# Optimization experiments

Measured on AMD Instinct MI355X. Metric: run time of the kernel, lower is better.

The kernel has to match this reference:

```python
import jax, jax.numpy as jnp
import numpy as np
from math import comb

ORDER = 16
K = ORDER + 1  # 17
D = 32         # input_dim
P = 20         # num_perm
N = 24576


def _bernstein(X, order):
    # X: [N, D] in [0,1] -> Bernstein basis [N, D, order+1]
    ks = jnp.arange(order + 1)
    binoms = jnp.array([comb(order, k) for k in range(order + 1)], jnp.float32)
    Xe = X[..., None]
    return (Xe ** ks) * ((1.0 - Xe) ** (order - ks)) * binoms


def _prior_sc_np(order):
    # prior_adjusting: sqrt(inv(B(x)^2) @ 1) at x = linspace(0,1,order+1)
    ks = np.arange(order + 1)
    binoms = np.array([comb(order, k) for k in range(order + 1)], np.float64)
    x = np.linspace(0.0, 1.0, order + 1)[:, None]
    B = (x ** ks) * ((1.0 - x) ** (order - ks)) * binoms  # (K, K)
    Pmat = np.linalg.inv(B ** 2)
    v = Pmat @ np.ones((order + 1, 1))
    return np.sqrt(np.maximum(v, 1e-12)).astype(np.float32)  # (K, 1)


def setup_inputs() -> dict:
    key = jax.random.key(0)
    k1, k2, k3, k4, k5 = jax.random.split(key, 5)
    mean_mu = (0.0001 / P) ** (1.0 / D)
    Xnew = jax.random.uniform(k1, (N, D), dtype=jnp.float32)
    meanw0 = mean_mu + 0.1 * jax.random.normal(k2, (P, 1, K), dtype=jnp.float32)
    meanw = mean_mu + 0.1 * jax.random.normal(k3, (D - 1, P, K, K), dtype=jnp.float32)
    varw0 = -0.1 + 0.1 * jax.random.normal(k4, (P, 1, K), dtype=jnp.float32)
    varw = -0.1 + 0.1 * jax.random.normal(k5, (D - 1, P, K, K), dtype=jnp.float32)
    rng = np.random.default_rng(0)
    perm = jnp.array(np.stack([rng.permutation(D) for _ in range(P)]), jnp.int32)
    prior_sc = jnp.array(_prior_sc_np(ORDER))
    post_prec = jnp.full((P,), float(P), dtype=jnp.float32)
    return {"Xnew": Xnew, "meanw0": meanw0, "meanw": meanw, "varw0": varw0,
            "varw": varw, "prior_sc": prior_sc, "post_prec": post_prec, "perm": perm}


def reference(Xnew, meanw0, meanw, varw0, varw, prior_sc, post_prec, perm):
    Bout = _bernstein(Xnew, ORDER)                      # (N, D, K)
    outB = jnp.transpose(Bout[:, perm], (1, 0, 2, 3))   # (P, N, D, K)
    outBd = jnp.transpose(outB, (2, 0, 1, 3))           # (D, P, N, K)

    # f_mean: ones(P,N,1) @ meanw0 -> broadcast of meanw0 rows; then chained small matmuls
    f0 = meanw0[:, 0, :][:, None, :] * outBd[0]         # (P, N, K)

    def mean_step(f, inputs):
        W, b = inputs                                   # W: (P,K,K), b: (P,N,K)
        return jnp.einsum('pnk,pkj->pnj', f, W) * b, None

    f, _ = jax.lax.scan(mean_step, f0, (meanw, outBd[1:]))
    f_mean = jnp.sum(jnp.sum(f, axis=-1), axis=0)[:, None]  # (N, 1)

    # f_var: weights exp(varw)*prior_sc^2.T, basis squared
    sc2 = (prior_sc ** 2)[:, 0]                          # (K,)
    g0 = (jnp.exp(varw0) * sc2)[:, 0, :][:, None, :] * outBd[0] ** 2  # (P, N, K)

    def var_step(g, inputs):
        Vw, b = inputs
        return jnp.einsum('pnk,pkj->pnj', g, jnp.exp(Vw) * sc2) * (b ** 2), None

    g, _ = jax.lax.scan(var_step, g0, (varw, outBd[1:]))
    f_var = jnp.sum(jnp.sum(g, axis=-1) / post_prec[:, None], axis=0)[:, None]  # (N, 1)
    return f_mean, f_var
```

## Files before the change

### kernel.cpp

```cpp
#include <hip/hip_runtime.h>

#define NN 24576
#define DD 32
#define KK 17
#define PP 20

__device__ __forceinline__ void bern17(float x, float* b) {
    const float binom[KK] = {1.f, 16.f, 120.f, 560.f, 1820.f, 4368.f, 8008.f, 11440.f,
                             12870.f, 11440.f, 8008.f, 4368.f, 1820.f, 560.f, 120.f, 16.f, 1.f};
    const float y = 1.0f - x;
    b[0] = 1.0f;
#pragma unroll
    for (int k = 1; k < KK; ++k) b[k] = b[k - 1] * x;
    float yp = 1.0f;
#pragma unroll
    for (int k = KK - 1; k >= 0; --k) {
        b[k] = b[k] * yp * binom[k];
        yp *= y;
    }
}

__global__ void prep_var(const float* __restrict__ varw, const float* __restrict__ varw0,
                         const float* __restrict__ prior_sc,
                         float* __restrict__ wv, float* __restrict__ wv0) {
    const int E1 = (DD - 1) * PP * KK * KK;
    int idx = blockIdx.x * blockDim.x + threadIdx.x;
    if (idx < E1) {
        int j = idx % KK;
        float s = prior_sc[j];
        wv[idx] = expf(varw[idx]) * s * s;
    } else if (idx < E1 + PP * KK) {
        int i = idx - E1;
        int k = i % KK;
        float s = prior_sc[k];
        wv0[i] = expf(varw0[i]) * s * s;
    }
}

__global__ void transpose_x(const float* __restrict__ X, float* __restrict__ XT) {
    __shared__ float t[32][33];
    const int n0 = blockIdx.x * 32;
    for (int r = threadIdx.y; r < 32; r += 8)
        t[r][threadIdx.x] = X[(n0 + r) * DD + threadIdx.x];
    __syncthreads();
    for (int d = threadIdx.y; d < 32; d += 8)
        XT[d * NN + n0 + threadIdx.x] = t[threadIdx.x][d];
}

__global__ __launch_bounds__(256, 4) void bez_chain2x2(
    const float* __restrict__ Xb,
    const float* __restrict__ mw0,
    const float* __restrict__ mW,
    const float* __restrict__ vw0,
    const float* __restrict__ vW,
    const float* __restrict__ post_prec,
    const int* __restrict__ perm,
    float* __restrict__ out)
{
    const bool VAR = (blockIdx.z != 0);
    const int p = blockIdx.y;
    const int n0 = blockIdx.x * 512 + threadIdx.x;
    const int n1 = n0 + 256;
    const int* __restrict__ pp = perm + p * DD;

    const float* __restrict__ w0 = (VAR ? vw0 : mw0);
    const float* __restrict__ W  = (VAR ? vW  : mW);

    float f0[KK], f1[KK], b0[KK], b1[KK];

    {
        const int pd = pp[0];
        const float x0 = Xb[pd * NN + n0];
        const float x1 = Xb[pd * NN + n1];
        bern17(x0, b0);
        bern17(x1, b1);
        if (VAR) {
#pragma unroll
            for (int k = 0; k < KK; ++k) { b0[k] *= b0[k]; b1[k] *= b1[k]; }
        }
        const float* __restrict__ w0p = w0 + p * KK;
#pragma unroll
        for (int k = 0; k < KK; ++k) { f0[k] = w0p[k] * b0[k]; f1[k] = w0p[k] * b1[k]; }
    }

    for (int d = 1; d < DD; ++d) {
        const int pd = pp[d];
        const float x0 = Xb[pd * NN + n0];
        const float x1 = Xb[pd * NN + n1];
        bern17(x0, b0);
        bern17(x1, b1);
        if (VAR) {
#pragma unroll
            for (int k = 0; k < KK; ++k) { b0[k] *= b0[k]; b1[k] *= b1[k]; }
        }

        const float* __restrict__ Wd = W + ((size_t)(d - 1) * PP + p) * (KK * KK);

        float fn0[KK], fn1[KK];
#pragma unroll
        for (int j = 0; j < KK; ++j) {
            const float w = Wd[j];
            fn0[j] = f0[0] * w;
            fn1[j] = f1[0] * w;
        }
#pragma unroll
        for (int k = 1; k < KK; ++k) {
            const float fk0 = f0[k];
            const float fk1 = f1[k];
#pragma unroll
            for (int j = 0; j < KK; ++j) {
                const float w = Wd[k * KK + j];
                fn0[j] = fmaf(fk0, w, fn0[j]);
                fn1[j] = fmaf(fk1, w, fn1[j]);
            }
        }
#pragma unroll
        for (int j = 0; j < KK; ++j) { f0[j] = fn0[j] * b0[j]; f1[j] = fn1[j] * b1[j]; }
    }

    float s0 = 0.0f, s1 = 0.0f;
#pragma unroll
    for (int j = 0; j < KK; ++j) { s0 += f0[j]; s1 += f1[j]; }
    if (VAR) { const float ip = 1.0f / post_prec[p]; s0 *= ip; s1 *= ip; }

    const int base = VAR ? NN : 0;
    atomicAdd(&out[base + n0], s0);
    atomicAdd(&out[base + n1], s1);
}

__global__ __launch_bounds__(256, 4) void bez_chain2(
    const float* __restrict__ Xb, const int sx_d, const int sx_n,
    const float* __restrict__ mw0, const float* __restrict__ mW,
    const float* __restrict__ vw0, const float* __restrict__ vW,
    const float* __restrict__ post_prec, const int* __restrict__ perm,
    float* __restrict__ out)
{
    const bool VAR = (blockIdx.z != 0);
    const int p = blockIdx.y;
    const int n = blockIdx.x * blockDim.x + threadIdx.x;
    const int* __restrict__ pp = perm + p * DD;
    const float* __restrict__ w0 = (VAR ? vw0 : mw0);
    const float* __restrict__ W  = (VAR ? vW  : mW);

    float f[KK], b[KK];
    {
        const int pd = pp[0];
        const float x = Xb[pd * sx_d + n * sx_n];
        bern17(x, b);
        if (VAR) {
#pragma unroll
            for (int k = 0; k < KK; ++k) b[k] *= b[k];
        }
        const float* __restrict__ w0p = w0 + p * KK;
#pragma unroll
        for (int k = 0; k < KK; ++k) f[k] = w0p[k] * b[k];
    }
    for (int d = 1; d < DD; ++d) {
        const int pd = pp[d];
        const float x = Xb[pd * sx_d + n * sx_n];
        bern17(x, b);
        if (VAR) {
#pragma unroll
            for (int k = 0; k < KK; ++k) b[k] *= b[k];
        }
        const float* __restrict__ Wd = W + ((size_t)(d - 1) * PP + p) * (KK * KK);
        float fn[KK];
#pragma unroll
        for (int j = 0; j < KK; ++j) fn[j] = 0.0f;
#pragma unroll
        for (int k = 0; k < KK; ++k) {
            const float fk = f[k];
#pragma unroll
            for (int j = 0; j < KK; ++j)
                fn[j] = fmaf(fk, Wd[k * KK + j], fn[j]);
        }
#pragma unroll
        for (int j = 0; j < KK; ++j) f[j] = fn[j] * b[j];
    }
    float s = 0.0f;
#pragma unroll
    for (int j = 0; j < KK; ++j) s += f[j];
    if (VAR) s /= post_prec[p];
    atomicAdd(&out[(VAR ? NN : 0) + n], s);
}

extern "C" void kernel_launch(void* const* d_in, const int* in_sizes, int n_in,
                              void* d_out, int out_size, void* d_ws, size_t ws_size,
                              hipStream_t stream) {
    const float* X    = (const float*)d_in[0];
    const float* mw0  = (const float*)d_in[1];
    const float* mw   = (const float*)d_in[2];
    const float* vw0  = (const float*)d_in[3];
    const float* vw   = (const float*)d_in[4];
    const float* psc  = (const float*)d_in[5];
    const float* ppr  = (const float*)d_in[6];
    const int*   perm = (const int*)d_in[7];
    float* out = (float*)d_out;

    const size_t wv_elems  = (size_t)(DD - 1) * PP * KK * KK;
    const size_t wv0_elems = (size_t)PP * KK;
    const size_t xt_elems  = (size_t)DD * NN;

    float* wv  = (float*)d_ws;
    float* wv0 = wv + wv_elems;
    float* XT  = wv0 + wv0_elems;

    const size_t need = (wv_elems + wv0_elems + xt_elems) * sizeof(float);
    const bool use_xt = (ws_size >= need);

    hipMemsetAsync(d_out, 0, (size_t)out_size * sizeof(float), stream);

    const int E = (DD - 1) * PP * KK * KK + PP * KK;
    prep_var<<<dim3((E + 255) / 256), dim3(256), 0, stream>>>(vw, vw0, psc, wv, wv0);

    if (use_xt) {
        transpose_x<<<dim3(NN / 32), dim3(32, 8), 0, stream>>>(X, XT);
        dim3 grid(NN / 512, PP, 2), blk(256);
        bez_chain2x2<<<grid, blk, 0, stream>>>(XT, mw0, mw, wv0, wv, ppr, perm, out);
    } else {
        dim3 grid(NN / 256, PP, 2), blk(256);
        bez_chain2<<<grid, blk, 0, stream>>>(X, 1, DD, mw0, mw, wv0, wv, ppr, perm, out);
    }
}
```

Measured before the change: 286.8 us.

## Fold binomial coefficients into weights and process four points per thread

The binomial coefficients of the Bernstein basis are moved out of the per-point basis evaluation and folded into the weight matrices, columnwise, in a prep kernel that now handles both the mean and variance weights. The main kernel now computes four points per thread instead of two, so each weight load is reused across more FMAs. The basis evaluation is placed after the matrix product to shorten live ranges. Occupancy is lowered to two blocks per CU to give room for the larger register footprint, which risks spilling or less latency hiding.

Result: slower. 879.1 us (+206.5%).

```diff
diff --git a/kernel.cpp b/kernel.cpp
--- a/kernel.cpp
+++ b/kernel.cpp
@@ -4,10 +4,169 @@
 #define DD 32
 #define KK 17
 #define PP 20
+#define WEU ((DD - 1) * PP * KK * KK)
+
+__device__ __forceinline__ float binom16(int k) {
+    const float b[KK] = {1.f, 16.f, 120.f, 560.f, 1820.f, 4368.f, 8008.f, 11440.f,
+                         12870.f, 11440.f, 8008.f, 4368.f, 1820.f, 560.f, 120.f, 16.f, 1.f};
+    return b[k];
+}
+
+__device__ __forceinline__ void bernT(float x, float* t) {
+    const float y = 1.0f - x;
+    t[0] = 1.0f;
+#pragma unroll
+    for (int k = 1; k < KK; ++k) t[k] = t[k - 1] * x;
+    float yp = y;
+#pragma unroll
+    for (int k = KK - 2; k >= 0; --k) {
+        t[k] *= yp;
+        yp *= y;
+    }
+}
+
+__global__ void prep_w_fold(const float* __restrict__ mw, const float* __restrict__ vw,
+                            const float* __restrict__ mw0, const float* __restrict__ vw0,
+                            const float* __restrict__ psc,
+                            float* __restrict__ Wm2, float* __restrict__ Wv2,
+                            float* __restrict__ w0m, float* __restrict__ w0v) {
+    int idx = blockIdx.x * blockDim.x + threadIdx.x;
+    if (idx < WEU) {
+        const int j = idx % KK;
+        Wm2[idx] = mw[idx] * binom16(j);
+    } else if (idx < 2 * WEU) {
+        const int i = idx - WEU;
+        const int j = i % KK;
+        const float s = psc[j] * binom16(j);
+        Wv2[i] = expf(vw[i]) * s * s;
+    } else if (idx < 2 * WEU + PP * KK) {
+        const int i = idx - 2 * WEU;
+        const int k = i % KK;
+        w0m[i] = mw0[i] * binom16(k);
+    } else if (idx < 2 * WEU + 2 * PP * KK) {
+        const int i = idx - 2 * WEU - PP * KK;
+        const int k = i % KK;
+        const float s = psc[k] * binom16(k);
+        w0v[i] = expf(vw0[i]) * s * s;
+    }
+}
+
+__global__ void transpose_x(const float* __restrict__ X, float* __restrict__ XT) {
+    __shared__ float t[32][33];
+    const int n0 = blockIdx.x * 32;
+    for (int r = threadIdx.y; r < 32; r += 8)
+        t[r][threadIdx.x] = X[(n0 + r) * DD + threadIdx.x];
+    __syncthreads();
+    for (int d = threadIdx.y; d < 32; d += 8)
+        XT[d * NN + n0 + threadIdx.x] = t[threadIdx.x][d];
+}
+
+__global__ __launch_bounds__(256, 2) void bez_chain4x(
+    const float* __restrict__ Xb,
+    const float* __restrict__ w0m,
+    const float* __restrict__ mW,
+    const float* __restrict__ w0v,
+    const float* __restrict__ vW,
+    const float* __restrict__ post_prec,
+    const int* __restrict__ perm,
+    float* __restrict__ out)
+{
+    const bool VAR = (blockIdx.z != 0);
+    const int p = blockIdx.y;
+    const int n0 = blockIdx.x * 1024 + threadIdx.x;
+    const int* __restrict__ pp = perm + p * DD;
+
+    const float* __restrict__ w0 = (VAR ? w0v : w0m);
+    const float* __restrict__ W  = (VAR ? vW  : mW);
+
+    float f0[KK], f1[KK], f2[KK], f3[KK];
+
+    {
+        const int pd = pp[0];
+        const float* __restrict__ xr = Xb + (size_t)pd * NN + n0;
+        float b0[KK], b1[KK], b2[KK], b3[KK];
+        bernT(xr[0], b0);
+        bernT(xr[256], b1);
+        bernT(xr[512], b2);
+        bernT(xr[768], b3);
+        if (VAR) {
+#pragma unroll
+            for (int k = 0; k < KK; ++k) {
+                b0[k] *= b0[k]; b1[k] *= b1[k]; b2[k] *= b2[k]; b3[k] *= b3[k];
+            }
+        }
+        const float* __restrict__ w0p = w0 + p * KK;
+#pragma unroll
+        for (int k = 0; k < KK; ++k) {
+            const float w = w0p[k];
+            f0[k] = w * b0[k]; f1[k] = w * b1[k]; f2[k] = w * b2[k]; f3[k] = w * b3[k];
+        }
+    }
+
+    for (int d = 1; d < DD; ++d) {
+        const int pd = pp[d];
+        const float* __restrict__ xr = Xb + (size_t)pd * NN + n0;
+        const float x0 = xr[0];
+        const float x1 = xr[256];
+        const float x2 = xr[512];
+        const float x3 = xr[768];
+
+        const float* __restrict__ Wd = W + ((size_t)(d - 1) * PP + p) * (KK * KK);
+
+        float fn0[KK], fn1[KK], fn2[KK], fn3[KK];
+#pragma unroll
+        for (int j = 0; j < KK; ++j) {
+            const float w = Wd[j];
+            fn0[j] = f0[0] * w; fn1[j] = f1[0] * w;
+            fn2[j] = f2[0] * w; fn3[j] = f3[0] * w;
+        }
+#pragma unroll
+        for (int k = 1; k < KK; ++k) {
+            const float a0 = f0[k], a1 = f1[k], a2 = f2[k], a3 = f3[k];
+#pragma unroll
+            for (int j = 0; j < KK; ++j) {
+                const float w = Wd[k * KK + j];
+                fn0[j] = fmaf(a0, w, fn0[j]);
+                fn1[j] = fmaf(a1, w, fn1[j]);
+                fn2[j] = fmaf(a2, w, fn2[j]);
+                fn3[j] = fmaf(a3, w, fn3[j]);
+            }
+        }
+
+        float b0[KK], b1[KK], b2[KK], b3[KK];
+        bernT(x0, b0);
+        bernT(x1, b1);
+        bernT(x2, b2);
+        bernT(x3, b3);
+        if (VAR) {
+#pragma unroll
+            for (int k = 0; k < KK; ++k) {
+                b0[k] *= b0[k]; b1[k] *= b1[k]; b2[k] *= b2[k]; b3[k] *= b3[k];
+            }
+        }
+#pragma unroll
+        for (int j = 0; j < KK; ++j) {
+            f0[j] = fn0[j] * b0[j]; f1[j] = fn1[j] * b1[j];
+            f2[j] = fn2[j] * b2[j]; f3[j] = fn3[j] * b3[j];
+        }
+    }
+
+    float s0 = 0.0f, s1 = 0.0f, s2 = 0.0f, s3 = 0.0f;
+#pragma unroll
+    for (int j = 0; j < KK; ++j) { s0 += f0[j]; s1 += f1[j]; s2 += f2[j]; s3 += f3[j]; }
+    if (VAR) {
+        const float ip = 1.0f / post_prec[p];
+        s0 *= ip; s1 *= ip; s2 *= ip; s3 *= ip;
+    }
+
+    const int base = (VAR ? NN : 0) + n0;
+    atomicAdd(&out[base], s0);
+    atomicAdd(&out[base + 256], s1);
+    atomicAdd(&out[base + 512], s2);
+    atomicAdd(&out[base + 768], s3);
+}
 
 __device__ __forceinline__ void bern17(float x, float* b) {
-    const float binom[KK] = {1.f, 16.f, 120.f, 560.f, 1820.f, 4368.f, 8008.f, 11440.f,
-                             12870.f, 11440.f, 8008.f, 4368.f, 1820.f, 560.f, 120.f, 16.f, 1.f};
     const float y = 1.0f - x;
     b[0] = 1.0f;
 #pragma unroll
@@ -15,7 +174,7 @@
     float yp = 1.0f;
 #pragma unroll
     for (int k = KK - 1; k >= 0; --k) {
-        b[k] = b[k] * yp * binom[k];
+        b[k] = b[k] * yp * binom16(k);
         yp *= y;
     }
 }
@@ -37,97 +196,6 @@
     }
 }
 
-__global__ void transpose_x(const float* __restrict__ X, float* __restrict__ XT) {
-    __shared__ float t[32][33];
-    const int n0 = blockIdx.x * 32;
-    for (int r = threadIdx.y; r < 32; r += 8)
-        t[r][threadIdx.x] = X[(n0 + r) * DD + threadIdx.x];
-    __syncthreads();
-    for (int d = threadIdx.y; d < 32; d += 8)
-        XT[d * NN + n0 + threadIdx.x] = t[threadIdx.x][d];
-}
-
-__global__ __launch_bounds__(256, 4) void bez_chain2x2(
-    const float* __restrict__ Xb,
-    const float* __restrict__ mw0,
-    const float* __restrict__ mW,
-    const float* __restrict__ vw0,
-    const float* __restrict__ vW,
-    const float* __restrict__ post_prec,
-    const int* __restrict__ perm,
-    float* __restrict__ out)
-{
-    const bool VAR = (blockIdx.z != 0);
-    const int p = blockIdx.y;
-    const int n0 = blockIdx.x * 512 + threadIdx.x;
-    const int n1 = n0 + 256;
-    const int* __restrict__ pp = perm + p * DD;
-
-    const float* __restrict__ w0 = (VAR ? vw0 : mw0);
-    const float* __restrict__ W  = (VAR ? vW  : mW);
-
-    float f0[KK], f1[KK], b0[KK], b1[KK];
-
-    {
-        const int pd = pp[0];
-        const float x0 = Xb[pd * NN + n0];
-        const float x1 = Xb[pd * NN + n1];
-        bern17(x0, b0);
-        bern17(x1, b1);
-        if (VAR) {
-#pragma unroll
-            for (int k = 0; k < KK; ++k) { b0[k] *= b0[k]; b1[k] *= b1[k]; }
-        }
-        const float* __restrict__ w0p = w0 + p * KK;
-#pragma unroll
-        for (int k = 0; k < KK; ++k) { f0[k] = w0p[k] * b0[k]; f1[k] = w0p[k] * b1[k]; }
-    }
-
-    for (int d = 1; d < DD; ++d) {
-        const int pd = pp[d];
-        const float x0 = Xb[pd * NN + n0];
-        const float x1 = Xb[pd * NN + n1];
-        bern17(x0, b0);
-        bern17(x1, b1);
-        if (VAR) {
-#pragma unroll
-            for (int k = 0; k < KK; ++k) { b0[k] *= b0[k]; b1[k] *= b1[k]; }
-        }
-
-        const float* __restrict__ Wd = W + ((size_t)(d - 1) * PP + p) * (KK * KK);
-
-        float fn0[KK], fn1[KK];
-#pragma unroll
-        for (int j = 0; j < KK; ++j) {
-            const float w = Wd[j];
-            fn0[j] = f0[0] * w;
-            fn1[j] = f1[0] * w;
-        }
-#pragma unroll
-        for (int k = 1; k < KK; ++k) {
-            const float fk0 = f0[k];
-            const float fk1 = f1[k];
-#pragma unroll
-            for (int j = 0; j < KK; ++j) {
-                const float w = Wd[k * KK + j];
-                fn0[j] = fmaf(fk0, w, fn0[j]);
-                fn1[j] = fmaf(fk1, w, fn1[j]);
-            }
-        }
-#pragma unroll
-        for (int j = 0; j < KK; ++j) { f0[j] = fn0[j] * b0[j]; f1[j] = fn1[j] * b1[j]; }
-    }
-
-    float s0 = 0.0f, s1 = 0.0f;
-#pragma unroll
-    for (int j = 0; j < KK; ++j) { s0 += f0[j]; s1 += f1[j]; }
-    if (VAR) { const float ip = 1.0f / post_prec[p]; s0 *= ip; s1 *= ip; }
-
-    const int base = VAR ? NN : 0;
-    atomicAdd(&out[base + n0], s0);
-    atomicAdd(&out[base + n1], s1);
-}
-
 __global__ __launch_bounds__(256, 4) void bez_chain2(
     const float* __restrict__ Xb, const int sx_d, const int sx_n,
     const float* __restrict__ mw0, const float* __restrict__ mW,
@@ -197,28 +265,44 @@
     const int*   perm = (const int*)d_in[7];
     float* out = (float*)d_out;
 
+    hipMemsetAsync(d_out, 0, (size_t)out_size * sizeof(float), stream);
+
+    const size_t xt_elems = (size_t)DD * NN;
+    const size_t need_main = ((size_t)2 * WEU + 2 * PP * KK + xt_elems) * sizeof(float);
+
+    if (ws_size >= need_main) {
+        float* Wm2 = (float*)d_ws;
+        float* Wv2 = Wm2 + WEU;
+        float* w0m = Wv2 + WEU;
+        float* w0v = w0m + PP * KK;
+        float* XT  = w0v + PP * KK;
+
+        const int E = 2 * WEU + 2 * PP * KK;
+        prep_w_fold<<<dim3((E + 255) / 256), dim3(256), 0, stream>>>(mw, vw, mw0, vw0, psc,
+                                                                     Wm2, Wv2, w0m, w0v);
+        transpose_x<<<dim3(NN / 32), dim3(32, 8), 0, stream>>>(X, XT);
+
+        dim3 grid(NN / 1024, PP, 2), blk(256);
+        bez_chain4x<<<grid, blk, 0, stream>>>(XT, w0m, Wm2, w0v, Wv2, ppr, perm, out);
+        return;
+    }
+
     const size_t wv_elems  = (size_t)(DD - 1) * PP * KK * KK;
     const size_t wv0_elems = (size_t)PP * KK;
-    const size_t xt_elems  = (size_t)DD * NN;
-
-    float* wv  = (float*)d_ws;
-    float* wv0 = wv + wv_elems;
-    float* XT  = wv0 + wv0_elems;
-
-    const size_t need = (wv_elems + wv0_elems + xt_elems) * sizeof(float);
-    const bool use_xt = (ws_size >= need);
-
-    hipMemsetAsync(d_out, 0, (size_t)out_size * sizeof(float), stream);
+    float* wv_b  = (float*)d_ws;
+    float* wv0_b = wv_b + wv_elems;
+    float* XT    = wv0_b + wv0_elems;
 
     const int E = (DD - 1) * PP * KK * KK + PP * KK;
-    prep_var<<<dim3((E + 255) / 256), dim3(256), 0, stream>>>(vw, vw0, psc, wv, wv0);
-
+    prep_var<<<dim3((E + 255) / 256), dim3(256), 0, stream>>>(vw, vw0, psc, wv_b, wv0_b);
+
+    const bool use_xt = ((wv_elems + wv0_elems + xt_elems) * sizeof(float) <= ws_size);
+    const float* Xb = X;
+    int sx_d = 1, sx_n = DD;
     if (use_xt) {
         transpose_x<<<dim3(NN / 32), dim3(32, 8), 0, stream>>>(X, XT);
-        dim3 grid(NN / 512, PP, 2), blk(256);
-        bez_chain2x2<<<grid, blk, 0, stream>>>(XT, mw0, mw, wv0, wv, ppr, perm, out);
-    } else {
-        dim3 grid(NN / 256, PP, 2), blk(256);
-        bez_chain2<<<grid, blk, 0, stream>>>(X, 1, DD, mw0, mw, wv0, wv, ppr, perm, out);
-    }
-}
+        Xb = XT; sx_d = NN; sx_n = 1;
+    }
+    dim3 grid(NN / 256, PP, 2), blk(256);
+    bez_chain2<<<grid, blk, 0, stream>>>(Xb, sx_d, sx_n, mw0, mw, wv0_b, wv_b, ppr, perm, out);
+}
```
